# Kernel tuning notes

Hardware: AMD Instinct MI355X
Metric: run time of the kernel (lower is better)

## Reference

```python
import jax, jax.numpy as jnp
import numpy as np

T, B, H, W, D, N, M, A = 48, 16, 16, 48, 684, 256, 256, 512
CQ, KQ, PAD = 512, 11, 5  # coverage conv: 1->512 channels, 11x11, pad 5


def setup_inputs() -> dict:
    key = jax.random.key(0)
    ks = iter(jax.random.split(key, 40))
    w = lambda *s: jax.random.normal(next(ks), s, jnp.float32) * 0.05
    inp = {
        "embedding": jax.random.normal(next(ks), (T, B, M), jnp.float32),
        "mask": jnp.ones((T, B), jnp.float32),
        "context": jax.random.normal(next(ks), (B, D, H, W), jnp.float32),
        "context_mask": jnp.ones((B, H, W), jnp.float32),
        "init_state": jax.random.normal(next(ks), (B, N), jnp.float32),
        # attention params
        "Ua_w": w(A, D), "Ua_b": w(A),              # conv_Ua (1x1 conv == linear over channels)
        "Wa_w": w(A, N),                              # fc_Wa (no bias)
        "Q_w": w(CQ, 1, KQ, KQ),                      # conv_Q (no bias)
        "Uf_w": w(A, CQ), "Uf_b": w(A),               # fc_Uf
        "va_w": w(1, A), "va_b": w(1),                # fc_va
        # GRU 1 (input-driven)
        "Wyz_w": w(N, M), "Wyz_b": w(N),
        "Wyr_w": w(N, M), "Wyr_b": w(N),
        "Wyh_w": w(N, M), "Wyh_b": w(N),
        "Uhz_w": w(N, N), "Uhr_w": w(N, N), "Uhh_w": w(N, N),
        # GRU 2 (context-driven)
        "Wcz_w": w(N, D), "Wcr_w": w(N, D), "Wch_w": w(N, D),
        "Uhz2_w": w(N, N), "Uhz2_b": w(N),
        "Uhr2_w": w(N, N), "Uhr2_b": w(N),
        "Uhh2_w": w(N, N), "Uhh2_b": w(N),
    }
    return inp


def reference(embedding, mask, context, context_mask, init_state,
              Ua_w, Ua_b, Wa_w, Q_w, Uf_w, Uf_b, va_w, va_b,
              Wyz_w, Wyz_b, Wyr_w, Wyr_b, Wyh_w, Wyh_b,
              Uhz_w, Uhr_w, Uhh_w, Wcz_w, Wcr_w, Wch_w,
              Uhz2_w, Uhz2_b, Uhr2_w, Uhr2_b, Uhh2_w, Uhh2_b):
    # Precompute, as the torch module does, the context projection and
    # embedding projections for all steps.
    Ua_ctx = jnp.einsum('bdhw,ad->hwba', context, Ua_w) + Ua_b   # [H,W,B,A]
    sz = jnp.einsum('tbm,nm->tbn', embedding, Wyz_w) + Wyz_b     # [T,B,N]
    sr = jnp.einsum('tbm,nm->tbn', embedding, Wyr_w) + Wyr_b
    sh = jnp.einsum('tbm,nm->tbn', embedding, Wyh_w) + Wyh_b
    ctx_mask_hwb = jnp.transpose(context_mask, (1, 2, 0))        # [H,W,B]
    nb = context.shape[0]
    alpha_past0 = jnp.zeros((nb, context.shape[2], context.shape[3]), context.dtype)

    def step(carry, xs):
        h, ap = carry
        m_t, sz_t, sr_t, sh_t = xs
        # GRU 1
        z1 = jax.nn.sigmoid(h @ Uhz_w.T + sz_t)
        r1 = jax.nn.sigmoid(h @ Uhr_w.T + sr_t)
        h1p = jnp.tanh((h @ Uhh_w.T) * r1 + sh_t)
        h1 = z1 * h + (1.0 - z1) * h1p
        h1 = m_t[:, None] * h1 + (1.0 - m_t)[:, None] * h
        # coverage-conv attention
        Wa_h1 = h1 @ Wa_w.T                                      # [B,A]
        cf = jax.lax.conv_general_dilated(
            ap[:, None], Q_w, (1, 1), [(PAD, PAD), (PAD, PAD)],
            dimension_numbers=('NCHW', 'OIHW', 'NCHW'))          # [B,CQ,H,W]
        cover = jnp.einsum('bchw,ac->hwba', cf, Uf_w) + Uf_b     # [H,W,B,A]
        att = jnp.tanh(Ua_ctx + Wa_h1[None, None] + cover)
        e = jnp.einsum('hwba,a->hwb', att, va_w[0]) + va_b[0]
        alpha = jnp.exp(e) * ctx_mask_hwb
        alpha = alpha / alpha.sum(axis=(0, 1))[None, None, :]    # normalize over H,W
        a_bhw = jnp.transpose(alpha, (2, 0, 1))
        ap_new = ap + a_bhw
        ct = jnp.einsum('bdhw,bhw->bd', context, a_bhw)          # [B,D]
        # GRU 2
        z2 = jax.nn.sigmoid(ct @ Wcz_w.T + h1 @ Uhz2_w.T + Uhz2_b)
        r2 = jax.nn.sigmoid(ct @ Wcr_w.T + h1 @ Uhr2_w.T + Uhr2_b)
        h2p = jnp.tanh(ct @ Wch_w.T + (h1 @ Uhh2_w.T + Uhh2_b) * r2)
        h2 = z2 * h1 + (1.0 - z2) * h2p
        h2 = m_t[:, None] * h2 + (1.0 - m_t)[:, None] * h1
        return (h2, ap_new), (h2, ct, a_bhw, ap_new)

    _, (h2ts, cts, alphas, alpha_pasts) = jax.lax.scan(
        step, (init_state, alpha_past0), (mask, sz, sr, sh))
    return h2ts, cts, alphas, alpha_pasts
```

## Files before the change

kernel.cpp:

```cpp
#include <hip/hip_runtime.h>
#include <hip/hip_bf16.h>
#include <stdint.h>

#define T_  48
#define B_  16
#define HW_ 768
#define D_  684
#define N_  256
#define A_  512

#define OFF_SZ     0u
#define OFF_SR     196608u
#define OFF_SH     393216u
#define OFF_UHZT   589824u
#define OFF_UHZ2T  786432u
#define OFF_G2HP   983040u
#define OFF_WAHP   1114112u
#define OFF_WAT    1179648u
#define OFF_WCZT   1310720u
#define OFF_UAT    1836032u
#define OFF_KCB    2186240u
#define OFF_G2CT   2219008u
#define OFF_H1     2251776u
#define OFF_AP     2275008u
#define OFF_AUN    2287296u
#define OFF_UACTX  2299584u

#define OUT_H2 0u
#define OUT_CT 196608u
#define OUT_AL 721920u
#define OUT_AP 1311744u

typedef __attribute__((ext_vector_type(8))) short bf16x8;
typedef __attribute__((ext_vector_type(16))) float floatx16;

__device__ __forceinline__ float sigf(float x)  { return 1.f / (1.f + __expf(-x)); }
__device__ __forceinline__ float tanhf_(float x){ float e = __expf(2.f*x); return 1.f - 2.f/(e + 1.f); }
__device__ __forceinline__ float bfval(unsigned short u){ return __uint_as_float(((unsigned)u) << 16); }
__device__ __forceinline__ unsigned short f2bf(float f){
  unsigned int x = __float_as_uint(f);
  return (unsigned short)((x + 0x7fffu + ((x >> 16) & 1u)) >> 16);
}

__global__ void k_prep(const float* __restrict__ Uhz, const float* __restrict__ Uhr, const float* __restrict__ Uhh,
                       const float* __restrict__ Uhz2, const float* __restrict__ Uhr2, const float* __restrict__ Uhh2,
                       const float* __restrict__ Wyz, const float* __restrict__ Wyr, const float* __restrict__ Wyh,
                       const float* __restrict__ Wa, const float* __restrict__ Wcz, const float* __restrict__ Wcr,
                       const float* __restrict__ Wch, const float* __restrict__ Ua, float* __restrict__ ws)
{
  int i = blockIdx.x * 256 + threadIdx.x;
  if (i < 589824) {
    int m = i >> 16, rem = i & 65535, r = rem >> 8, c = rem & 255;
    const float* s;
    unsigned dst;
    switch (m) { case 0: s=Uhz;  dst=OFF_UHZT;            break;
                 case 1: s=Uhr;  dst=OFF_UHZT+65536u;     break;
                 case 2: s=Uhh;  dst=OFF_UHZT+131072u;    break;
                 case 3: s=Uhz2; dst=OFF_UHZ2T;           break;
                 case 4: s=Uhr2; dst=OFF_UHZ2T+65536u;    break;
                 case 5: s=Uhh2; dst=OFF_UHZ2T+131072u;   break;
                 case 6: s=Wyz;  dst=OFF_G2HP;            break;
                 case 7: s=Wyr;  dst=OFF_G2HP+65536u;     break;
                 default: s=Wyh; dst=OFF_WAHP;            break;}
    ws[dst + c*256 + r] = s[rem];
  } else if (i < 720896) {
    int j = i - 589824, r = j >> 8, c = j & 255;
    ws[OFF_WAT + c*512 + r] = Wa[j];
  } else if (i < 1246208) {
    int j = i - 720896; int m = j / 175104; int rem = j - m*175104;
    int r = rem / 684, c = rem - r*684;
    const float* s = (m == 0) ? Wcz : (m == 1) ? Wcr : Wch;
    ws[OFF_WCZT + m*175104 + c*256 + r] = s[rem];
  } else if (i < 1596416) {
    int j = i - 1246208; int r = j / 684, c = j - r*684;
    ws[OFF_UAT + c*512 + r] = Ua[j];
  } else if (i < 1608704) {
    ws[OFF_AP + (i - 1596416)] = 0.f;
  }
}

__global__ void k_kcomb(const float* __restrict__ Uf, const float* __restrict__ Qw, float* __restrict__ ws)
{
  __shared__ float s_uf[16 * 516];
  int tid = threadIdx.x, a0 = blockIdx.x * 16;
  for (int i = tid; i < 16 * 512; i += 256) { int al = i >> 9, c = i & 511; s_uf[al*516 + c] = Uf[(a0 + al)*512 + c]; }
  __syncthreads();
  int al = tid & 15, kb = tid >> 4;
  unsigned short* kcb = (unsigned short*)(ws + OFF_KCB);
  for (int kk = kb; kk < 128; kk += 16) {
    float acc = 0.f;
    if (kk < 121) {
      #pragma unroll 8
      for (int c = 0; c < 512; ++c) acc += s_uf[al*516 + c] * Qw[c*121 + kk];
    }
    kcb[(size_t)(a0 + al)*128 + kk] = f2bf(acc);
  }
}

__global__ void k_embproj(const float* __restrict__ emb, const float* __restrict__ bz,
                          const float* __restrict__ br, const float* __restrict__ bh,
                          float* __restrict__ ws)
{
  __shared__ __align__(16) float s_e[256 * 16];
  int tid = threadIdx.x, row0 = blockIdx.x * 16;
  for (int i = tid; i < 4096; i += 256) { int r = i >> 8, m = i & 255; s_e[m*16 + r] = emb[(row0 + r)*256 + m]; }
  __syncthreads();
  int n = tid;
  float az[16], arr[16], ahh[16];
  float vz = bz[n], vr = br[n], vh = bh[n];
  #pragma unroll
  for (int r = 0; r < 16; ++r) { az[r] = vz; arr[r] = vr; ahh[r] = vh; }
  for (int m = 0; m < 256; ++m) {
    float wz = ws[OFF_G2HP + m*256 + n];
    float wr = ws[OFF_G2HP + 65536u + m*256 + n];
    float wh = ws[OFF_WAHP + m*256 + n];
    #pragma unroll
    for (int r = 0; r < 16; ++r) { float e = s_e[m*16 + r]; az[r] += wz*e; arr[r] += wr*e; ahh[r] += wh*e; }
  }
  #pragma unroll
  for (int r = 0; r < 16; ++r) {
    int ro = (row0 + r)*256 + n;
    ws[OFF_SZ + ro] = az[r]; ws[OFF_SR + ro] = arr[r]; ws[OFF_SH + ro] = ahh[r];
  }
}

__global__ void __launch_bounds__(512) k_uactx(const float* __restrict__ ctx, float* __restrict__ ws)
{
  __shared__ __align__(16) float s_c[684 * 16];
  int tid = threadIdx.x;
  int b = blockIdx.x / 48, chunk = blockIdx.x % 48, hw0 = chunk * 16;
  for (int i = tid; i < 684*16; i += 512) {
    int d = i >> 4, r = i & 15;
    s_c[i] = ctx[((size_t)(b*684 + d))*768 + hw0 + r];
  }
  __syncthreads();
  int a = tid;
  float acc[16];
  #pragma unroll
  for (int r = 0; r < 16; ++r) acc[r] = 0.f;
  const float* uat = ws + OFF_UAT;
  for (int d = 0; d < 684; ++d) {
    float wv = uat[d*512 + a];
    const float4* cp = (const float4*)(s_c + d*16);
    float4 c0 = cp[0], c1 = cp[1], c2 = cp[2], c3 = cp[3];
    acc[0]  += wv*c0.x; acc[1]  += wv*c0.y; acc[2]  += wv*c0.z; acc[3]  += wv*c0.w;
    acc[4]  += wv*c1.x; acc[5]  += wv*c1.y; acc[6]  += wv*c1.z; acc[7]  += wv*c1.w;
    acc[8]  += wv*c2.x; acc[9]  += wv*c2.y; acc[10] += wv*c2.z; acc[11] += wv*c2.w;
    acc[12] += wv*c3.x; acc[13] += wv*c3.y; acc[14] += wv*c3.z; acc[15] += wv*c3.w;
  }
  unsigned short* up = (unsigned short*)(ws + OFF_UACTX);
  #pragma unroll
  for (int r = 0; r < 16; ++r) up[((size_t)(b*768 + hw0 + r))*512 + a] = f2bf(acc[r]);
}

__global__ void __launch_bounds__(256) k_step1(int t, const float* __restrict__ inits, const float* __restrict__ maskp,
                                               const float* __restrict__ bz2, const float* __restrict__ br2,
                                               const float* __restrict__ bh2,
                                               float* __restrict__ out, float* __restrict__ ws)
{
  __shared__ float s_h[256];
  __shared__ float s_part[3][8][32];
  __shared__ float s_h1[32];
  int tid = threadIdx.x;
  int b = blockIdx.x >> 3, q = blockIdx.x & 7;
  {
    int n = tid;
    float hv;
    if (t == 0) {
      hv = inits[b*256 + n];
    } else {
      float h1v = ws[OFF_H1 + b*256 + n];
      float gz = ws[OFF_G2CT + (b*3 + 0)*256 + n];
      float gr = ws[OFF_G2CT + (b*3 + 1)*256 + n];
      float gc = ws[OFF_G2CT + (b*3 + 2)*256 + n];
      float gu = 0.f;
      #pragma unroll
      for (int qq = 0; qq < 8; ++qq) {
        gz += ws[OFF_G2HP + (size_t)((b*8 + qq)*3 + 0)*256 + n];
        gr += ws[OFF_G2HP + (size_t)((b*8 + qq)*3 + 1)*256 + n];
        gu += ws[OFF_G2HP + (size_t)((b*8 + qq)*3 + 2)*256 + n];
      }
      float z2 = sigf(gz + bz2[n]);
      float r2 = sigf(gr + br2[n]);
      float h2p = tanhf_(gc + (gu + bh2[n]) * r2);
      float h2 = z2*h1v + (1.f - z2)*h2p;
      float m = maskp[(t-1)*16 + b];
      hv = m*h2 + (1.f - m)*h1v;
      if (q == 0) out[OUT_H2 + (size_t)((t-1)*16 + b)*256 + n] = hv;
    }
    s_h[n] = hv;
  }
  if (q == 0) for (int i = tid; i < 768; i += 256) ws[OFF_AUN + b*768 + i] = 0.f;
  __syncthreads();
  {
    int nl = tid & 31, kq = tid >> 5;
    int col = q*32 + nl;
    const float* Wz = ws + OFF_UHZT;
    const float* Wr = ws + OFF_UHZT + 65536u;
    const float* Wh = ws + OFF_UHZT + 131072u;
    float a0 = 0.f, a1 = 0.f, a2 = 0.f;
    #pragma unroll 8
    for (int k = kq*32; k < kq*32 + 32; ++k) {
      float hk = s_h[k];
      a0 += Wz[k*256 + col]*hk; a1 += Wr[k*256 + col]*hk; a2 += Wh[k*256 + col]*hk;
    }
    s_part[0][kq][nl] = a0; s_part[1][kq][nl] = a1; s_part[2][kq][nl] = a2;
  }
  __syncthreads();
  if (tid < 32) {
    float g0 = 0.f, g1 = 0.f, g2 = 0.f;
    #pragma unroll
    for (int j = 0; j < 8; ++j) { g0 += s_part[0][j][tid]; g1 += s_part[1][j][tid]; g2 += s_part[2][j][tid]; }
    int col = q*32 + tid;
    int ro = (t*16 + b)*256 + col;
    float z1 = sigf(g0 + ws[OFF_SZ + ro]);
    float r1 = sigf(g1 + ws[OFF_SR + ro]);
    float h1p = tanhf_(g2 * r1 + ws[OFF_SH + ro]);
    float m = maskp[t*16 + b];
    float h = s_h[col];
    float h1 = m*(z1*h + (1.f - z1)*h1p) + (1.f - m)*h;
    s_h1[tid] = h1;
    ws[OFF_H1 + b*256 + col] = h1;
  }
  __syncthreads();
  {
    float acc0 = 0.f, acc1 = 0.f;
    #pragma unroll 8
    for (int j = 0; j < 32; ++j) {
      float h1j = s_h1[j];
      acc0 += ws[OFF_WAT + (q*32 + j)*512 + tid]       * h1j;
      acc1 += ws[OFF_WAT + (q*32 + j)*512 + tid + 256] * h1j;
    }
    ws[OFF_WAHP + (size_t)(b*8 + q)*512 + tid]       = acc0;
    ws[OFF_WAHP + (size_t)(b*8 + q)*512 + tid + 256] = acc1;
  }
  #pragma unroll
  for (int g = 0; g < 3; ++g) {
    const float* Wb = ws + OFF_UHZ2T + g*65536u;
    float acc = 0.f;
    #pragma unroll 8
    for (int j = 0; j < 32; ++j) acc += Wb[(q*32 + j)*256 + tid] * s_h1[j];
    ws[OFF_G2HP + (size_t)((b*8 + q)*3 + g)*256 + tid] = acc;
  }
}

__global__ void __launch_bounds__(256) k_cover(const float* __restrict__ va,
                                               const float* __restrict__ Uab, const float* __restrict__ Ufb,
                                               float* __restrict__ ws)
{
  __shared__ unsigned short sA[64 * 136];
  __shared__ float sWah[512];
  __shared__ float sVa[512];
  int tid = threadIdx.x;
  int blk = blockIdx.x;
  int b = blk / 24; int chA = blk % 24; int mt = chA >> 1; int nt2 = chA & 1;
  for (int i = tid; i < 512; i += 256) {
    float v = Uab[i] + Ufb[i];
    #pragma unroll
    for (int qq = 0; qq < 8; ++qq) v += ws[OFF_WAHP + (size_t)(b*8 + qq)*512 + i];
    sWah[i] = v; sVa[i] = va[i];
  }
  if (chA == 0) for (int i = tid; i < 768; i += 256) ws[OFF_G2CT + b*768 + i] = 0.f;
  const float* ap = ws + OFF_AP + b*768;
  for (int idx = tid; idx < 64*128; idx += 256) {
    int r = idx & 63, k = idx >> 6;
    int hw = mt*64 + r; int hh = hw / 48; int wwp = hw - hh*48;
    float v = 0.f;
    if (k < 121) {
      int kh = k / 11, kw = k - kh*11;
      int shh = hh + kh - 5, sww = wwp + kw - 5;
      if (shh >= 0 && shh < 16 && sww >= 0 && sww < 48) v = ap[shh*48 + sww];
    }
    sA[r*136 + k] = f2bf(v);
  }
  __syncthreads();
  int lane = tid & 63; int w = tid >> 6; int mw = w >> 1; int nw = w & 1;
  int c5 = lane & 31; int q = lane >> 5;
  bf16x8 af[8];
  {
    int m = mw*32 + c5;
    #pragma unroll
    for (int ks = 0; ks < 8; ++ks)
      af[ks] = *(const bf16x8*)(sA + m*136 + ks*16 + q*8);
  }
  const unsigned short* kct = (const unsigned short*)(ws + OFF_KCB);
  const unsigned short* uact = (const unsigned short*)(ws + OFF_UACTX);
  float e_part[16];
  #pragma unroll
  for (int r = 0; r < 16; ++r) e_part[r] = 0.f;

  for (int sp = 0; sp < 2; ++sp) {
    int n_base = nt2*256 + nw*128 + sp*64;
    floatx16 acc[2];
    #pragma unroll
    for (int r = 0; r < 16; ++r) { acc[0][r] = 0.f; acc[1][r] = 0.f; }
    const bf16x8* kb0 = (const bf16x8*)(kct + (size_t)(n_base + c5)*128 + q*8);
    const bf16x8* kb1 = (const bf16x8*)(kct + (size_t)(n_base + 32 + c5)*128 + q*8);
    #pragma unroll
    for (int ks = 0; ks < 8; ++ks) {
      bf16x8 b0 = kb0[ks*2];
      bf16x8 b1 = kb1[ks*2];
      acc[0] = __builtin_amdgcn_mfma_f32_32x32x16_bf16(af[ks], b0, acc[0], 0, 0, 0);
      acc[1] = __builtin_amdgcn_mfma_f32_32x32x16_bf16(af[ks], b1, acc[1], 0, 0, 0);
    }
    #pragma unroll
    for (int half = 0; half < 2; ++half) {
      int col = n_base + half*32 + c5;
      float vav = sVa[col], wah = sWah[col];
      #pragma unroll
      for (int r = 0; r < 16; ++r) {
        int row32 = (r & 3) + 8*(r >> 2) + 4*q;
        int hw = mt*64 + mw*32 + row32;
        float x = acc[half][r] + wah + bfval(uact[((size_t)(b*768 + hw))*512 + col]);
        e_part[r] += vav * tanhf_(x);
      }
    }
  }
  #pragma unroll
  for (int r = 0; r < 16; ++r) {
    float v = e_part[r];
    v += __shfl_xor(v, 1); v += __shfl_xor(v, 2); v += __shfl_xor(v, 4);
    v += __shfl_xor(v, 8); v += __shfl_xor(v, 16);
    e_part[r] = v;
  }
  if (c5 == 0) {
    #pragma unroll
    for (int r = 0; r < 16; ++r) {
      int row32 = (r & 3) + 8*(r >> 2) + 4*q;
      int hw = mt*64 + mw*32 + row32;
      atomicAdd(&ws[OFF_AUN + b*768 + hw], e_part[r]);
    }
  }
}

__global__ void __launch_bounds__(256) k_alpha(int t, const float* __restrict__ ctx, const float* __restrict__ cmask,
                                               const float* __restrict__ vab,
                                               float* __restrict__ out, float* __restrict__ ws)
{
  __shared__ __align__(16) float s_al[768];
  __shared__ float s_red[4];
  __shared__ float s_ct[32];
  int tid = threadIdx.x;
  int b = blockIdx.x / 22, dc = blockIdx.x % 22;
  float vb = vab[0];
  float local = 0.f;
  for (int i = tid; i < 768; i += 256) {
    float e = ws[OFF_AUN + b*768 + i] + vb;
    float un = __expf(e) * cmask[b*768 + i];
    s_al[i] = un; local += un;
  }
  local += __shfl_xor(local, 1); local += __shfl_xor(local, 2); local += __shfl_xor(local, 4);
  local += __shfl_xor(local, 8); local += __shfl_xor(local, 16); local += __shfl_xor(local, 32);
  if ((tid & 63) == 0) s_red[tid >> 6] = local;
  __syncthreads();
  float inv = 1.f / (s_red[0] + s_red[1] + s_red[2] + s_red[3]);
  if (dc == 0) {
    float* outA = out + OUT_AL + (size_t)(t*16 + b)*768;
    float* outP = out + OUT_AP + (size_t)(t*16 + b)*768;
    for (int i = tid; i < 768; i += 256) {
      float av = s_al[i] * inv;
      float np = ws[OFF_AP + b*768 + i] + av;
      ws[OFF_AP + b*768 + i] = np;
      outA[i] = av; outP[i] = np;
    }
  }
  {
    int dl = tid >> 3, qq = tid & 7;
    int d = dc*32 + dl;
    if (d < 684) {
      const float4* cp  = (const float4*)(ctx + ((size_t)(b*684 + d))*768);
      const float4* alp = (const float4*)s_al;
      float s = 0.f;
      #pragma unroll 8
      for (int i = 0; i < 24; ++i) {
        float4 cv = cp[i*8 + qq]; float4 av = alp[i*8 + qq];
        s += cv.x*av.x + cv.y*av.y + cv.z*av.z + cv.w*av.w;
      }
      s += __shfl_xor(s, 1); s += __shfl_xor(s, 2); s += __shfl_xor(s, 4);
      s *= inv;
      if (qq == 0) {
        out[OUT_CT + (size_t)(t*16 + b)*684 + d] = s;
        s_ct[dl] = s;
      }
    } else if (qq == 0) {
      s_ct[dl] = 0.f;
    }
  }
  __syncthreads();
  {
    int d0 = dc*32;
    int jm = 684 - d0; if (jm > 32) jm = 32;
    #pragma unroll
    for (int g = 0; g < 3; ++g) {
      const float* Wb = ws + OFF_WCZT + g*175104u;
      float acc = 0.f;
      for (int j = 0; j < jm; ++j) acc += Wb[(d0 + j)*256 + tid] * s_ct[j];
      atomicAdd(&ws[OFF_G2CT + (size_t)(b*3 + g)*256 + tid], acc);
    }
  }
}

__global__ void k_final(const float* __restrict__ maskp, const float* __restrict__ bz2,
                        const float* __restrict__ br2, const float* __restrict__ bh2,
                        float* __restrict__ out, float* __restrict__ ws)
{
  int b = blockIdx.x, n = threadIdx.x;
  float h1v = ws[OFF_H1 + b*256 + n];
  float gz = ws[OFF_G2CT + (b*3 + 0)*256 + n];
  float gr = ws[OFF_G2CT + (b*3 + 1)*256 + n];
  float gc = ws[OFF_G2CT + (b*3 + 2)*256 + n];
  float gu = 0.f;
  #pragma unroll
  for (int qq = 0; qq < 8; ++qq) {
    gz += ws[OFF_G2HP + (size_t)((b*8 + qq)*3 + 0)*256 + n];
    gr += ws[OFF_G2HP + (size_t)((b*8 + qq)*3 + 1)*256 + n];
    gu += ws[OFF_G2HP + (size_t)((b*8 + qq)*3 + 2)*256 + n];
  }
  float z2 = sigf(gz + bz2[n]);
  float r2 = sigf(gr + br2[n]);
  float h2p = tanhf_(gc + (gu + bh2[n]) * r2);
  float h2 = z2*h1v + (1.f - z2)*h2p;
  float m = maskp[47*16 + b];
  out[OUT_H2 + (size_t)(47*16 + b)*256 + n] = m*h2 + (1.f - m)*h1v;
}

extern "C" void kernel_launch(void* const* d_in, const int* in_sizes, int n_in,
                              void* d_out, int out_size, void* d_ws, size_t ws_size,
                              hipStream_t stream)
{
  const float* emb   = (const float*)d_in[0];
  const float* maskp = (const float*)d_in[1];
  const float* ctx   = (const float*)d_in[2];
  const float* cmask = (const float*)d_in[3];
  const float* inits = (const float*)d_in[4];
  const float* Ua    = (const float*)d_in[5];
  const float* Uab   = (const float*)d_in[6];
  const float* Wa    = (const float*)d_in[7];
  const float* Qw    = (const float*)d_in[8];
  const float* Uf    = (const float*)d_in[9];
  const float* Ufb   = (const float*)d_in[10];
  const float* va    = (const float*)d_in[11];
  const float* vab   = (const float*)d_in[12];
  const float* Wyz   = (const float*)d_in[13];
  const float* Wyzb  = (const float*)d_in[14];
  const float* Wyr   = (const float*)d_in[15];
  const float* Wyrb  = (const float*)d_in[16];
  const float* Wyh   = (const float*)d_in[17];
  const float* Wyhb  = (const float*)d_in[18];
  const float* Uhz   = (const float*)d_in[19];
  const float* Uhr   = (const float*)d_in[20];
  const float* Uhh   = (const float*)d_in[21];
  const float* Wcz   = (const float*)d_in[22];
  const float* Wcr   = (const float*)d_in[23];
  const float* Wch   = (const float*)d_in[24];
  const float* Uhz2  = (const float*)d_in[25];
  const float* Uhz2b = (const float*)d_in[26];
  const float* Uhr2  = (const float*)d_in[27];
  const float* Uhr2b = (const float*)d_in[28];
  const float* Uhh2  = (const float*)d_in[29];
  const float* Uhh2b = (const float*)d_in[30];
  float* out = (float*)d_out;
  float* ws  = (float*)d_ws;

  k_prep<<<dim3(6284), dim3(256), 0, stream>>>(Uhz, Uhr, Uhh, Uhz2, Uhr2, Uhh2,
                                               Wyz, Wyr, Wyh, Wa, Wcz, Wcr, Wch, Ua, ws);
  k_kcomb<<<dim3(32), dim3(256), 0, stream>>>(Uf, Qw, ws);
  k_embproj<<<dim3(48), dim3(256), 0, stream>>>(emb, Wyzb, Wyrb, Wyhb, ws);
  k_uactx<<<dim3(768), dim3(512), 0, stream>>>(ctx, ws);

  for (int t = 0; t < 48; ++t) {
    k_step1<<<dim3(128), dim3(256), 0, stream>>>(t, inits, maskp, Uhz2b, Uhr2b, Uhh2b, out, ws);
    k_cover<<<dim3(384), dim3(256), 0, stream>>>(va, Uab, Ufb, ws);
    k_alpha<<<dim3(352), dim3(256), 0, stream>>>(t, ctx, cmask, vab, out, ws);
  }
  k_final<<<dim3(16), dim3(256), 0, stream>>>(maskp, Uhz2b, Uhr2b, Uhh2b, out, ws);
  (void)in_sizes; (void)n_in; (void)out_size; (void)ws_size;
}
```

Measured before the change: 2.770 ms.

## Fuse GRU step into alpha kernel via last-block counter; MFMA context projection

Removes the per-step k_step1 launch. The last k_alpha block for each batch, found with an atomic counter, finishes GRU2, then runs GRU1 and the Wa/Uhz2 projections for the next step and clears the accumulators. This cuts the per-step launches from three to two. The one-off Ua·context projection is rewritten to use bf16 MFMA with a pre-transposed bf16 Ua, and k_kcomb is parallelised one block per kernel tap. In exchange, the serial tail of each step now runs on only 16 blocks, and the context projection loses precision from bf16 inputs.

Result: slower. 7.399 ms (+167.2%).

```diff
diff --git a/kernel.cpp b/kernel.cpp
--- a/kernel.cpp
+++ b/kernel.cpp
@@ -14,11 +14,12 @@
 #define OFF_SH     393216u
 #define OFF_UHZT   589824u
 #define OFF_UHZ2T  786432u
-#define OFF_G2HP   983040u
-#define OFF_WAHP   1114112u
+#define OFF_G2H    983040u
+#define OFF_CTR    995328u
+#define OFF_WAH    1114112u
 #define OFF_WAT    1179648u
 #define OFF_WCZT   1310720u
-#define OFF_UAT    1836032u
+#define OFF_UAB    1836032u
 #define OFF_KCB    2186240u
 #define OFF_G2CT   2219008u
 #define OFF_H1     2251776u
@@ -53,15 +54,15 @@
     int m = i >> 16, rem = i & 65535, r = rem >> 8, c = rem & 255;
     const float* s;
     unsigned dst;
-    switch (m) { case 0: s=Uhz;  dst=OFF_UHZT;            break;
-                 case 1: s=Uhr;  dst=OFF_UHZT+65536u;     break;
-                 case 2: s=Uhh;  dst=OFF_UHZT+131072u;    break;
-                 case 3: s=Uhz2; dst=OFF_UHZ2T;           break;
-                 case 4: s=Uhr2; dst=OFF_UHZ2T+65536u;    break;
-                 case 5: s=Uhh2; dst=OFF_UHZ2T+131072u;   break;
-                 case 6: s=Wyz;  dst=OFF_G2HP;            break;
-                 case 7: s=Wyr;  dst=OFF_G2HP+65536u;     break;
-                 default: s=Wyh; dst=OFF_WAHP;            break;}
+    switch (m) { case 0: s=Uhz;  dst=OFF_UHZT;           break;
+                 case 1: s=Uhr;  dst=OFF_UHZT+65536u;    break;
+                 case 2: s=Uhh;  dst=OFF_UHZT+131072u;   break;
+                 case 3: s=Uhz2; dst=OFF_UHZ2T;          break;
+                 case 4: s=Uhr2; dst=OFF_UHZ2T+65536u;   break;
+                 case 5: s=Uhh2; dst=OFF_UHZ2T+131072u;  break;
+                 case 6: s=Wyz;  dst=983040u;            break;
+                 case 7: s=Wyr;  dst=1048576u;           break;
+                 default: s=Wyh; dst=1114112u;           break;}
     ws[dst + c*256 + r] = s[rem];
   } else if (i < 720896) {
     int j = i - 589824, r = j >> 8, c = j & 255;
@@ -72,28 +73,39 @@
     const float* s = (m == 0) ? Wcz : (m == 1) ? Wcr : Wch;
     ws[OFF_WCZT + m*175104 + c*256 + r] = s[rem];
   } else if (i < 1596416) {
-    int j = i - 1246208; int r = j / 684, c = j - r*684;
-    ws[OFF_UAT + c*512 + r] = Ua[j];
-  } else if (i < 1608704) {
-    ws[OFF_AP + (i - 1596416)] = 0.f;
-  }
-}
-
-__global__ void k_kcomb(const float* __restrict__ Uf, const float* __restrict__ Qw, float* __restrict__ ws)
-{
-  __shared__ float s_uf[16 * 516];
-  int tid = threadIdx.x, a0 = blockIdx.x * 16;
-  for (int i = tid; i < 16 * 512; i += 256) { int al = i >> 9, c = i & 511; s_uf[al*516 + c] = Uf[(a0 + al)*512 + c]; }
-  __syncthreads();
-  int al = tid & 15, kb = tid >> 4;
+    int j = i - 1246208; int a = j / 684, d = j - a*684;
+    unsigned short* uab = (unsigned short*)(ws + OFF_UAB);
+    uab[(size_t)a*688 + d] = f2bf(Ua[j]);
+  } else if (i < 1598464) {
+    int j = i - 1596416; int a = j >> 2, d = 684 + (j & 3);
+    unsigned short* uab = (unsigned short*)(ws + OFF_UAB);
+    uab[(size_t)a*688 + d] = 0;
+  } else if (i < 1610752) {
+    ws[OFF_AP + (i - 1598464)] = 0.f;
+  }
+}
+
+__global__ void __launch_bounds__(256) k_kcomb(const float* __restrict__ Uf, const float* __restrict__ Qw,
+                                               float* __restrict__ ws)
+{
   unsigned short* kcb = (unsigned short*)(ws + OFF_KCB);
-  for (int kk = kb; kk < 128; kk += 16) {
+  int tid = threadIdx.x, k = blockIdx.x;
+  if (k >= 121) {
+    for (int a = tid; a < 512; a += 256) kcb[(size_t)a*128 + k] = 0;
+    return;
+  }
+  __shared__ float sQ[512];
+  for (int c = tid; c < 512; c += 256) sQ[c] = Qw[c*121 + k];
+  __syncthreads();
+  int rl = tid >> 5, cl = tid & 31;
+  for (int r0 = 0; r0 < 512; r0 += 8) {
+    int a = r0 + rl;
     float acc = 0.f;
-    if (kk < 121) {
-      #pragma unroll 8
-      for (int c = 0; c < 512; ++c) acc += s_uf[al*516 + c] * Qw[c*121 + kk];
-    }
-    kcb[(size_t)(a0 + al)*128 + kk] = f2bf(acc);
+    #pragma unroll 4
+    for (int c = cl; c < 512; c += 32) acc += Uf[(size_t)a*512 + c] * sQ[c];
+    acc += __shfl_xor(acc, 1); acc += __shfl_xor(acc, 2); acc += __shfl_xor(acc, 4);
+    acc += __shfl_xor(acc, 8); acc += __shfl_xor(acc, 16);
+    if (cl == 0) kcb[(size_t)a*128 + k] = f2bf(acc);
   }
 }
 
@@ -111,9 +123,9 @@
   #pragma unroll
   for (int r = 0; r < 16; ++r) { az[r] = vz; arr[r] = vr; ahh[r] = vh; }
   for (int m = 0; m < 256; ++m) {
-    float wz = ws[OFF_G2HP + m*256 + n];
-    float wr = ws[OFF_G2HP + 65536u + m*256 + n];
-    float wh = ws[OFF_WAHP + m*256 + n];
+    float wz = ws[983040u + m*256 + n];
+    float wr = ws[1048576u + m*256 + n];
+    float wh = ws[1114112u + m*256 + n];
     #pragma unroll
     for (int r = 0; r < 16; ++r) { float e = s_e[m*16 + r]; az[r] += wz*e; arr[r] += wr*e; ahh[r] += wh*e; }
   }
@@ -124,129 +136,100 @@
   }
 }
 
-__global__ void __launch_bounds__(512) k_uactx(const float* __restrict__ ctx, float* __restrict__ ws)
-{
-  __shared__ __align__(16) float s_c[684 * 16];
+__global__ void __launch_bounds__(256) k_uactx(const float* __restrict__ ctx, float* __restrict__ ws)
+{
+  __shared__ unsigned short sA[64 * 24];
   int tid = threadIdx.x;
-  int b = blockIdx.x / 48, chunk = blockIdx.x % 48, hw0 = chunk * 16;
-  for (int i = tid; i < 684*16; i += 512) {
-    int d = i >> 4, r = i & 15;
-    s_c[i] = ctx[((size_t)(b*684 + d))*768 + hw0 + r];
-  }
-  __syncthreads();
-  int a = tid;
-  float acc[16];
-  #pragma unroll
-  for (int r = 0; r < 16; ++r) acc[r] = 0.f;
-  const float* uat = ws + OFF_UAT;
-  for (int d = 0; d < 684; ++d) {
-    float wv = uat[d*512 + a];
-    const float4* cp = (const float4*)(s_c + d*16);
-    float4 c0 = cp[0], c1 = cp[1], c2 = cp[2], c3 = cp[3];
-    acc[0]  += wv*c0.x; acc[1]  += wv*c0.y; acc[2]  += wv*c0.z; acc[3]  += wv*c0.w;
-    acc[4]  += wv*c1.x; acc[5]  += wv*c1.y; acc[6]  += wv*c1.z; acc[7]  += wv*c1.w;
-    acc[8]  += wv*c2.x; acc[9]  += wv*c2.y; acc[10] += wv*c2.z; acc[11] += wv*c2.w;
-    acc[12] += wv*c3.x; acc[13] += wv*c3.y; acc[14] += wv*c3.z; acc[15] += wv*c3.w;
+  int b = blockIdx.x / 12, ch = blockIdx.x % 12, hw0 = ch * 64;
+  const unsigned short* uab = (const unsigned short*)(ws + OFF_UAB);
+  int lane = tid & 63, w = tid >> 6, mw = w >> 1, nw = w & 1;
+  int c5 = lane & 31, q = lane >> 5;
+  int m = mw*32 + c5;
+  int nb = nw*256;
+  floatx16 acc[8];
+  #pragma unroll
+  for (int nt = 0; nt < 8; ++nt)
+    #pragma unroll
+    for (int r = 0; r < 16; ++r) acc[nt][r] = 0.f;
+  int dd = tid >> 4, iw = tid & 15;
+  for (int kt = 0; kt < 43; ++kt) {
+    int d = kt*16 + dd;
+    float4 v = {0.f, 0.f, 0.f, 0.f};
+    if (d < 684) v = *(const float4*)(ctx + ((size_t)(b*684 + d))*768 + hw0 + iw*4);
+    __syncthreads();
+    sA[(iw*4 + 0)*24 + dd] = f2bf(v.x);
+    sA[(iw*4 + 1)*24 + dd] = f2bf(v.y);
+    sA[(iw*4 + 2)*24 + dd] = f2bf(v.z);
+    sA[(iw*4 + 3)*24 + dd] = f2bf(v.w);
+    __syncthreads();
+    bf16x8 af = *(const bf16x8*)(sA + m*24 + q*8);
+    #pragma unroll
+    for (int nt = 0; nt < 8; ++nt) {
+      bf16x8 bf = *(const bf16x8*)(uab + (size_t)(nb + nt*32 + c5)*688 + kt*16 + q*8);
+      acc[nt] = __builtin_amdgcn_mfma_f32_32x32x16_bf16(af, bf, acc[nt], 0, 0, 0);
+    }
   }
   unsigned short* up = (unsigned short*)(ws + OFF_UACTX);
   #pragma unroll
-  for (int r = 0; r < 16; ++r) up[((size_t)(b*768 + hw0 + r))*512 + a] = f2bf(acc[r]);
-}
-
-__global__ void __launch_bounds__(256) k_step1(int t, const float* __restrict__ inits, const float* __restrict__ maskp,
-                                               const float* __restrict__ bz2, const float* __restrict__ br2,
-                                               const float* __restrict__ bh2,
-                                               float* __restrict__ out, float* __restrict__ ws)
-{
-  __shared__ float s_h[256];
-  __shared__ float s_part[3][8][32];
-  __shared__ float s_h1[32];
-  int tid = threadIdx.x;
-  int b = blockIdx.x >> 3, q = blockIdx.x & 7;
-  {
-    int n = tid;
-    float hv;
-    if (t == 0) {
-      hv = inits[b*256 + n];
-    } else {
-      float h1v = ws[OFF_H1 + b*256 + n];
-      float gz = ws[OFF_G2CT + (b*3 + 0)*256 + n];
-      float gr = ws[OFF_G2CT + (b*3 + 1)*256 + n];
-      float gc = ws[OFF_G2CT + (b*3 + 2)*256 + n];
-      float gu = 0.f;
-      #pragma unroll
-      for (int qq = 0; qq < 8; ++qq) {
-        gz += ws[OFF_G2HP + (size_t)((b*8 + qq)*3 + 0)*256 + n];
-        gr += ws[OFF_G2HP + (size_t)((b*8 + qq)*3 + 1)*256 + n];
-        gu += ws[OFF_G2HP + (size_t)((b*8 + qq)*3 + 2)*256 + n];
-      }
-      float z2 = sigf(gz + bz2[n]);
-      float r2 = sigf(gr + br2[n]);
-      float h2p = tanhf_(gc + (gu + bh2[n]) * r2);
-      float h2 = z2*h1v + (1.f - z2)*h2p;
-      float m = maskp[(t-1)*16 + b];
-      hv = m*h2 + (1.f - m)*h1v;
-      if (q == 0) out[OUT_H2 + (size_t)((t-1)*16 + b)*256 + n] = hv;
-    }
-    s_h[n] = hv;
-  }
-  if (q == 0) for (int i = tid; i < 768; i += 256) ws[OFF_AUN + b*768 + i] = 0.f;
-  __syncthreads();
-  {
-    int nl = tid & 31, kq = tid >> 5;
-    int col = q*32 + nl;
-    const float* Wz = ws + OFF_UHZT;
-    const float* Wr = ws + OFF_UHZT + 65536u;
-    const float* Wh = ws + OFF_UHZT + 131072u;
-    float a0 = 0.f, a1 = 0.f, a2 = 0.f;
-    #pragma unroll 8
-    for (int k = kq*32; k < kq*32 + 32; ++k) {
-      float hk = s_h[k];
-      a0 += Wz[k*256 + col]*hk; a1 += Wr[k*256 + col]*hk; a2 += Wh[k*256 + col]*hk;
-    }
-    s_part[0][kq][nl] = a0; s_part[1][kq][nl] = a1; s_part[2][kq][nl] = a2;
-  }
-  __syncthreads();
-  if (tid < 32) {
-    float g0 = 0.f, g1 = 0.f, g2 = 0.f;
-    #pragma unroll
-    for (int j = 0; j < 8; ++j) { g0 += s_part[0][j][tid]; g1 += s_part[1][j][tid]; g2 += s_part[2][j][tid]; }
-    int col = q*32 + tid;
-    int ro = (t*16 + b)*256 + col;
-    float z1 = sigf(g0 + ws[OFF_SZ + ro]);
-    float r1 = sigf(g1 + ws[OFF_SR + ro]);
-    float h1p = tanhf_(g2 * r1 + ws[OFF_SH + ro]);
-    float m = maskp[t*16 + b];
-    float h = s_h[col];
-    float h1 = m*(z1*h + (1.f - z1)*h1p) + (1.f - m)*h;
-    s_h1[tid] = h1;
-    ws[OFF_H1 + b*256 + col] = h1;
-  }
-  __syncthreads();
-  {
-    float acc0 = 0.f, acc1 = 0.f;
-    #pragma unroll 8
-    for (int j = 0; j < 32; ++j) {
-      float h1j = s_h1[j];
-      acc0 += ws[OFF_WAT + (q*32 + j)*512 + tid]       * h1j;
-      acc1 += ws[OFF_WAT + (q*32 + j)*512 + tid + 256] * h1j;
-    }
-    ws[OFF_WAHP + (size_t)(b*8 + q)*512 + tid]       = acc0;
-    ws[OFF_WAHP + (size_t)(b*8 + q)*512 + tid + 256] = acc1;
-  }
-  #pragma unroll
-  for (int g = 0; g < 3; ++g) {
-    const float* Wb = ws + OFF_UHZ2T + g*65536u;
-    float acc = 0.f;
-    #pragma unroll 8
-    for (int j = 0; j < 32; ++j) acc += Wb[(q*32 + j)*256 + tid] * s_h1[j];
-    ws[OFF_G2HP + (size_t)((b*8 + q)*3 + g)*256 + tid] = acc;
-  }
-}
-
-__global__ void __launch_bounds__(256) k_cover(const float* __restrict__ va,
+  for (int nt = 0; nt < 8; ++nt) {
+    int col = nb + nt*32 + c5;
+    #pragma unroll
+    for (int r = 0; r < 16; ++r) {
+      int row32 = (r & 3) + 8*(r >> 2) + 4*q;
+      int hw = hw0 + mw*32 + row32;
+      up[((size_t)(b*768 + hw))*512 + col] = f2bf(acc[nt][r]);
+    }
+  }
+}
+
+__global__ void __launch_bounds__(256) k_step0(const float* __restrict__ inits, const float* __restrict__ maskp,
                                                const float* __restrict__ Uab, const float* __restrict__ Ufb,
                                                float* __restrict__ ws)
+{
+  __shared__ float s_h[256], s_h1[256];
+  int b = blockIdx.x, n = threadIdx.x;
+  s_h[n] = inits[b*256 + n];
+  __syncthreads();
+  {
+    float z = ws[OFF_SZ + (0*16 + b)*256 + n], r = ws[OFF_SR + (0*16 + b)*256 + n];
+    float sh = ws[OFF_SH + (0*16 + b)*256 + n], uh = 0.f;
+    #pragma unroll 4
+    for (int k = 0; k < 256; ++k) {
+      float hk = s_h[k];
+      z  += ws[OFF_UHZT + k*256 + n] * hk;
+      r  += ws[OFF_UHZT + 65536u + k*256 + n] * hk;
+      uh += ws[OFF_UHZT + 131072u + k*256 + n] * hk;
+    }
+    float z1 = sigf(z), r1 = sigf(r);
+    float h1p = tanhf_(uh * r1 + sh);
+    float m = maskp[0*16 + b];
+    float h = s_h[n];
+    float h1 = m*(z1*h + (1.f - z1)*h1p) + (1.f - m)*h;
+    s_h1[n] = h1;
+    ws[OFF_H1 + b*256 + n] = h1;
+  }
+  __syncthreads();
+  #pragma unroll
+  for (int half = 0; half < 2; ++half) {
+    int a = n + half*256;
+    float acc = 0.f;
+    #pragma unroll 4
+    for (int k = 0; k < 256; ++k) acc += ws[OFF_WAT + k*512 + a] * s_h1[k];
+    ws[OFF_WAH + b*512 + a] = acc + Uab[a] + Ufb[a];
+  }
+  #pragma unroll
+  for (int g = 0; g < 3; ++g) {
+    float acc = 0.f;
+    #pragma unroll 4
+    for (int k = 0; k < 256; ++k) acc += ws[OFF_UHZ2T + g*65536u + k*256 + n] * s_h1[k];
+    ws[OFF_G2H + (b*3 + g)*256 + n] = acc;
+  }
+  for (int i = n; i < 768; i += 256) ws[OFF_AUN + b*768 + i] = 0.f;
+  for (int i = n; i < 768; i += 256) ws[OFF_G2CT + b*768 + i] = 0.f;
+  if (n == 0) ((unsigned*)(ws + OFF_CTR))[b] = 0u;
+}
+
+__global__ void __launch_bounds__(256) k_cover(const float* __restrict__ va, float* __restrict__ ws)
 {
   __shared__ unsigned short sA[64 * 136];
   __shared__ float sWah[512];
@@ -254,13 +237,7 @@
   int tid = threadIdx.x;
   int blk = blockIdx.x;
   int b = blk / 24; int chA = blk % 24; int mt = chA >> 1; int nt2 = chA & 1;
-  for (int i = tid; i < 512; i += 256) {
-    float v = Uab[i] + Ufb[i];
-    #pragma unroll
-    for (int qq = 0; qq < 8; ++qq) v += ws[OFF_WAHP + (size_t)(b*8 + qq)*512 + i];
-    sWah[i] = v; sVa[i] = va[i];
-  }
-  if (chA == 0) for (int i = tid; i < 768; i += 256) ws[OFF_G2CT + b*768 + i] = 0.f;
+  for (int i = tid; i < 512; i += 256) { sWah[i] = ws[OFF_WAH + b*512 + i]; sVa[i] = va[i]; }
   const float* ap = ws + OFF_AP + b*768;
   for (int idx = tid; idx < 64*128; idx += 256) {
     int r = idx & 63, k = idx >> 6;
@@ -334,12 +311,16 @@
 }
 
 __global__ void __launch_bounds__(256) k_alpha(int t, const float* __restrict__ ctx, const float* __restrict__ cmask,
-                                               const float* __restrict__ vab,
+                                               const float* __restrict__ vab, const float* __restrict__ maskp,
+                                               const float* __restrict__ Uab, const float* __restrict__ Ufb,
+                                               const float* __restrict__ bz2, const float* __restrict__ br2,
+                                               const float* __restrict__ bh2,
                                                float* __restrict__ out, float* __restrict__ ws)
 {
   __shared__ __align__(16) float s_al[768];
   __shared__ float s_red[4];
   __shared__ float s_ct[32];
+  __shared__ int s_last;
   int tid = threadIdx.x;
   int b = blockIdx.x / 22, dc = blockIdx.x % 22;
   float vb = vab[0];
@@ -398,30 +379,75 @@
       atomicAdd(&ws[OFF_G2CT + (size_t)(b*3 + g)*256 + tid], acc);
     }
   }
-}
-
-__global__ void k_final(const float* __restrict__ maskp, const float* __restrict__ bz2,
-                        const float* __restrict__ br2, const float* __restrict__ bh2,
-                        float* __restrict__ out, float* __restrict__ ws)
-{
-  int b = blockIdx.x, n = threadIdx.x;
-  float h1v = ws[OFF_H1 + b*256 + n];
-  float gz = ws[OFF_G2CT + (b*3 + 0)*256 + n];
-  float gr = ws[OFF_G2CT + (b*3 + 1)*256 + n];
-  float gc = ws[OFF_G2CT + (b*3 + 2)*256 + n];
-  float gu = 0.f;
-  #pragma unroll
-  for (int qq = 0; qq < 8; ++qq) {
-    gz += ws[OFF_G2HP + (size_t)((b*8 + qq)*3 + 0)*256 + n];
-    gr += ws[OFF_G2HP + (size_t)((b*8 + qq)*3 + 1)*256 + n];
-    gu += ws[OFF_G2HP + (size_t)((b*8 + qq)*3 + 2)*256 + n];
-  }
-  float z2 = sigf(gz + bz2[n]);
-  float r2 = sigf(gr + br2[n]);
-  float h2p = tanhf_(gc + (gu + bh2[n]) * r2);
-  float h2 = z2*h1v + (1.f - z2)*h2p;
-  float m = maskp[47*16 + b];
-  out[OUT_H2 + (size_t)(47*16 + b)*256 + n] = m*h2 + (1.f - m)*h1v;
+  __syncthreads();
+  if (tid == 0) {
+    unsigned* ctr = (unsigned*)(ws + OFF_CTR);
+    unsigned c = __hip_atomic_fetch_add(&ctr[b], 1u, __ATOMIC_ACQ_REL, __HIP_MEMORY_SCOPE_AGENT);
+    s_last = (c == (unsigned)(22*t + 21)) ? 1 : 0;
+  }
+  __syncthreads();
+  if (!s_last) return;
+  float* s_h  = s_al;
+  float* s_h1 = s_al + 256;
+  int n = tid;
+  float* g2ct = ws + OFF_G2CT;
+  {
+    float h1v = ws[OFF_H1 + b*256 + n];
+    float gz = __hip_atomic_load(&g2ct[(b*3 + 0)*256 + n], __ATOMIC_RELAXED, __HIP_MEMORY_SCOPE_AGENT);
+    float gr = __hip_atomic_load(&g2ct[(b*3 + 1)*256 + n], __ATOMIC_RELAXED, __HIP_MEMORY_SCOPE_AGENT);
+    float gc = __hip_atomic_load(&g2ct[(b*3 + 2)*256 + n], __ATOMIC_RELAXED, __HIP_MEMORY_SCOPE_AGENT);
+    gz += ws[OFF_G2H + (b*3 + 0)*256 + n];
+    gr += ws[OFF_G2H + (b*3 + 1)*256 + n];
+    float gu = ws[OFF_G2H + (b*3 + 2)*256 + n];
+    float z2 = sigf(gz + bz2[n]);
+    float r2 = sigf(gr + br2[n]);
+    float h2p = tanhf_(gc + (gu + bh2[n]) * r2);
+    float h2 = z2*h1v + (1.f - z2)*h2p;
+    float m = maskp[t*16 + b];
+    float hv = m*h2 + (1.f - m)*h1v;
+    out[OUT_H2 + (size_t)(t*16 + b)*256 + n] = hv;
+    s_h[n] = hv;
+  }
+  if (t >= 47) return;
+  __syncthreads();
+  {
+    int ro = ((t+1)*16 + b)*256 + n;
+    float z = ws[OFF_SZ + ro], r = ws[OFF_SR + ro], sh = ws[OFF_SH + ro], uh = 0.f;
+    #pragma unroll 4
+    for (int k = 0; k < 256; ++k) {
+      float hk = s_h[k];
+      z  += ws[OFF_UHZT + k*256 + n] * hk;
+      r  += ws[OFF_UHZT + 65536u + k*256 + n] * hk;
+      uh += ws[OFF_UHZT + 131072u + k*256 + n] * hk;
+    }
+    float z1 = sigf(z), r1 = sigf(r);
+    float h1p = tanhf_(uh * r1 + sh);
+    float m = maskp[(t+1)*16 + b];
+    float h = s_h[n];
+    float h1 = m*(z1*h + (1.f - z1)*h1p) + (1.f - m)*h;
+    s_h1[n] = h1;
+    ws[OFF_H1 + b*256 + n] = h1;
+  }
+  __syncthreads();
+  #pragma unroll
+  for (int half = 0; half < 2; ++half) {
+    int a = n + half*256;
+    float acc = 0.f;
+    #pragma unroll 4
+    for (int k = 0; k < 256; ++k) acc += ws[OFF_WAT + k*512 + a] * s_h1[k];
+    ws[OFF_WAH + b*512 + a] = acc + Uab[a] + Ufb[a];
+  }
+  #pragma unroll
+  for (int g = 0; g < 3; ++g) {
+    float acc = 0.f;
+    #pragma unroll 4
+    for (int k = 0; k < 256; ++k) acc += ws[OFF_UHZ2T + g*65536u + k*256 + n] * s_h1[k];
+    ws[OFF_G2H + (b*3 + g)*256 + n] = acc;
+  }
+  for (int i = n; i < 768; i += 256) ws[OFF_AUN + b*768 + i] = 0.f;
+  #pragma unroll
+  for (int g = 0; g < 3; ++g)
+    __hip_atomic_store(&g2ct[(b*3 + g)*256 + n], 0.f, __ATOMIC_RELAXED, __HIP_MEMORY_SCOPE_AGENT);
 }
 
 extern "C" void kernel_launch(void* const* d_in, const int* in_sizes, int n_in,
@@ -462,17 +488,17 @@
   float* out = (float*)d_out;
   float* ws  = (float*)d_ws;
 
-  k_prep<<<dim3(6284), dim3(256), 0, stream>>>(Uhz, Uhr, Uhh, Uhz2, Uhr2, Uhh2,
+  k_prep<<<dim3(6292), dim3(256), 0, stream>>>(Uhz, Uhr, Uhh, Uhz2, Uhr2, Uhh2,
                                                Wyz, Wyr, Wyh, Wa, Wcz, Wcr, Wch, Ua, ws);
-  k_kcomb<<<dim3(32), dim3(256), 0, stream>>>(Uf, Qw, ws);
+  k_kcomb<<<dim3(128), dim3(256), 0, stream>>>(Uf, Qw, ws);
   k_embproj<<<dim3(48), dim3(256), 0, stream>>>(emb, Wyzb, Wyrb, Wyhb, ws);
-  k_uactx<<<dim3(768), dim3(512), 0, stream>>>(ctx, ws);
+  k_uactx<<<dim3(192), dim3(256), 0, stream>>>(ctx, ws);
+  k_step0<<<dim3(16), dim3(256), 0, stream>>>(inits, maskp, Uab, Ufb, ws);
 
   for (int t = 0; t < 48; ++t) {
-    k_step1<<<dim3(128), dim3(256), 0, stream>>>(t, inits, maskp, Uhz2b, Uhr2b, Uhh2b, out, ws);
-    k_cover<<<dim3(384), dim3(256), 0, stream>>>(va, Uab, Ufb, ws);
-    k_alpha<<<dim3(352), dim3(256), 0, stream>>>(t, ctx, cmask, vab, out, ws);
-  }
-  k_final<<<dim3(16), dim3(256), 0, stream>>>(maskp, Uhz2b, Uhr2b, Uhh2b, out, ws);
+    k_cover<<<dim3(384), dim3(256), 0, stream>>>(va, ws);
+    k_alpha<<<dim3(352), dim3(256), 0, stream>>>(t, ctx, cmask, vab, maskp,
+                                                 Uab, Ufb, Uhz2b, Uhr2b, Uhh2b, out, ws);
+  }
   (void)in_sizes; (void)n_in; (void)out_size; (void)ws_size;
 }
```
